# Optimization experiments

Hardware: AMD Instinct MI355X
Metric: run time of the kernel (lower is better)

## Reference

```python
import jax, jax.numpy as jnp
import numpy as np

B, S, D, H = 4, 2048, 1024, 16
DEPTH = D // H
NEG = -1000000000.0


def setup_inputs() -> dict:
    key = jax.random.key(0)
    ks = jax.random.split(key, 11)
    scale = 1.0 / np.sqrt(D)
    return {
        "q": jax.random.normal(ks[0], (B, S, D), jnp.float32),
        "k": jax.random.normal(ks[1], (B, S, D), jnp.float32),
        "v": jax.random.normal(ks[2], (B, S, D), jnp.float32),
        "wq_w": jax.random.normal(ks[3], (D, D), jnp.float32) * scale,
        "wq_b": jax.random.normal(ks[4], (D,), jnp.float32) * 0.01,
        "wk_w": jax.random.normal(ks[5], (D, D), jnp.float32) * scale,
        "wk_b": jax.random.normal(ks[6], (D,), jnp.float32) * 0.01,
        "wv_w": jax.random.normal(ks[7], (D, D), jnp.float32) * scale,
        "wv_b": jax.random.normal(ks[8], (D,), jnp.float32) * 0.01,
        "dense_w": jax.random.normal(ks[9], (D, D), jnp.float32) * scale,
        "dense_b": jax.random.normal(ks[10], (D,), jnp.float32) * 0.01,
    }


def _split_heads(x):
    # (B, S, D) -> (B, H, S, depth)
    b, s, _ = x.shape
    return x.reshape(b, s, H, DEPTH).transpose(0, 2, 1, 3)


def reference(q, k, v, wq_w, wq_b, wk_w, wk_b, wv_w, wv_b, dense_w, dense_b):
    b, s, _ = q.shape
    qh = _split_heads(q @ wq_w.T + wq_b)
    kh = _split_heads(k @ wk_w.T + wk_b)
    vh = _split_heads(v @ wv_w.T + wv_b)
    logits = jnp.einsum('bhqd,bhkd->bhqk', qh, kh) / np.sqrt(DEPTH).astype(np.float32)
    # additive causal mask (strict upper triangle = -1e9)
    mask = jnp.where(jnp.triu(jnp.ones((s, s), jnp.float32), k=1) == 1.0, NEG, 0.0)
    logits = logits + mask
    attn = jax.nn.softmax(logits, axis=-1)
    out = jnp.einsum('bhqk,bhkd->bhqd', attn, vh)
    out = out.transpose(0, 2, 1, 3).reshape(b, s, D)
    return out @ dense_w.T + dense_b
```

## Files before the change

kernel.cpp:

```cpp
#include <hip/hip_runtime.h>
#include <hip/hip_bf16.h>


typedef __attribute__((ext_vector_type(8))) short bf16x8;
typedef __attribute__((ext_vector_type(4))) float f32x4;
typedef __attribute__((ext_vector_type(8))) unsigned short u16x8;

#define MFMA16(a, b, c) __builtin_amdgcn_mfma_f32_16x16x32_bf16(a, b, c, 0, 0, 0)

#define GLOAD_LDS16(gp, lp)                                                    \
  __builtin_amdgcn_global_load_lds(                                            \
      (const __attribute__((address_space(1))) void*)(gp),                     \
      (__attribute__((address_space(3))) void*)(lp), 16, 0, 0)

__device__ __forceinline__ unsigned short f2bf(float f) {
  union { float f; unsigned u; } x; x.f = f;
  unsigned u = x.u;
  return (unsigned short)((u + 0x7fffu + ((u >> 16) & 1u)) >> 16);
}

__device__ __forceinline__ unsigned pk2(float a, float b) {
  union { __hip_bfloat162 h; unsigned u; } cv;
  cv.h = __float22bfloat162_rn(float2{a, b});
  return cv.u;
}

__global__ __launch_bounds__(256) void convert_kernel(
    const float* __restrict__ q, const float* __restrict__ k,
    const float* __restrict__ v, const float* __restrict__ wq,
    const float* __restrict__ wk, const float* __restrict__ wv,
    const float* __restrict__ wd, const float* __restrict__ bq,
    const float* __restrict__ bk, const float* __restrict__ bv,
    unsigned short* __restrict__ dst, float* __restrict__ bias_pack) {
  const size_t tid0 = (size_t)blockIdx.x * blockDim.x + threadIdx.x;
  const size_t nthreads = (size_t)gridDim.x * blockDim.x;
  if (tid0 < 3072) {
    bias_pack[tid0] = tid0 < 1024 ? bq[tid0]
                     : (tid0 < 2048 ? bk[tid0 - 1024] : bv[tid0 - 2048]);
  }
  const size_t NQ = 8192ull * 1024;
  const size_t NW = 1024ull * 1024;
  const size_t total_chunks = (3 * NQ + 4 * NW) / 8;
  for (size_t c = tid0; c < total_chunks; c += nthreads) {
    const size_t e = c * 8;
    const float* src;
    if (e < NQ) src = q + e;
    else if (e < 2 * NQ) src = k + (e - NQ);
    else if (e < 3 * NQ) src = v + (e - 2 * NQ);
    else {
      const size_t we = e - 3 * NQ;
      if (we < NW) src = wq + we;
      else if (we < 2 * NW) src = wk + (we - NW);
      else if (we < 3 * NW) src = wv + (we - 2 * NW);
      else src = wd + (we - 3 * NW);
    }
    f32x4 a = *(const f32x4*)(src);
    f32x4 b = *(const f32x4*)(src + 4);
    u16x8 o;
    o[0] = f2bf(a[0]); o[1] = f2bf(a[1]); o[2] = f2bf(a[2]); o[3] = f2bf(a[3]);
    o[4] = f2bf(b[0]); o[5] = f2bf(b[1]); o[6] = f2bf(b[2]); o[7] = f2bf(b[3]);
    *(u16x8*)(dst + e) = o;
  }
}

template <int MODE>
__global__ __launch_bounds__(512, 2) void gemm8_kernel(
    const unsigned short* __restrict__ Abase,
    const unsigned short* __restrict__ Wbase,
    const float* __restrict__ biasbase, unsigned short* __restrict__ dstb,
    float* __restrict__ dstf) {
  __shared__ __attribute__((aligned(16))) unsigned short Ablk[3][128 * 64];
  __shared__ __attribute__((aligned(16))) unsigned short Bblk[3][256 * 64];
  const size_t NQ = 8192ull * 1024, NW = 1024ull * 1024;
  const int nx = gridDim.x, ny = gridDim.y;
  const int tot = nx * ny * (int)gridDim.z;
  int flat = ((int)blockIdx.z * ny + blockIdx.y) * nx + blockIdx.x;
  flat = (flat & 7) * (tot >> 3) + (flat >> 3);
  const int bx = flat % nx;
  const int tmp = flat / nx;
  const int by = tmp % ny;
  const int z = tmp / ny;

  const unsigned short* A;
  const unsigned short* W;
  if (MODE == 0) { A = Abase + (size_t)z * NQ; W = Wbase + (size_t)z * NW; }
  else if (MODE == 2) { A = Wbase + 2 * NW; W = Abase + 2 * NQ; }
  else { A = Abase; W = Wbase; }
  const int m0 = by * 128, n0 = bx * 256;

  const int tid = threadIdx.x, lane = tid & 63, w = tid >> 6;
  const int wm = w >> 2, wn = w & 3;
  const int llo = lane & 15, lhi = lane >> 4;

  int srcA[2], srcB[4];
#pragma unroll
  for (int j = 0; j < 4; ++j) {
    const int c = tid + j * 512;
    const int off = (c >> 3) * 1024 + ((((c & 7) ^ ((c >> 3) & 7))) << 3);
    if (j < 2) srcA[j] = off;
    srcB[j] = off;
  }
  const unsigned short* Ag = A + (size_t)m0 * 1024;
  const unsigned short* Wg = W + (size_t)n0 * 1024;

#define STA(bi, kt_, j)                                                        \
  GLOAD_LDS16(Ag + srcA[j] + (kt_) * 64,                                       \
              (unsigned short*)Ablk[bi] + (tid + (j) * 512) * 8)
#define STB(bi, kt_, j)                                                        \
  GLOAD_LDS16(Wg + srcB[j] + (kt_) * 64,                                       \
              (unsigned short*)Bblk[bi] + (tid + (j) * 512) * 8)

  f32x4 acc[4][4] = {};
  const int cswz0 = ((lhi ^ (llo & 7)) << 3);
  const int cswz1 = (((4 + lhi) ^ (llo & 7)) << 3);

  STA(0, 0, 0); STA(0, 0, 1);
  STB(0, 0, 0); STB(0, 0, 1); STB(0, 0, 2); STB(0, 0, 3);
  STA(1, 1, 0); STA(1, 1, 1);
  STB(1, 1, 0); STB(1, 1, 1); STB(1, 1, 2); STB(1, 1, 3);

#pragma unroll
  for (int kt = 0; kt < 16; ++kt) {
    const int cb = kt % 3, nb = (kt + 2) % 3;
    __builtin_amdgcn_s_barrier();
    __builtin_amdgcn_sched_barrier(0);
    if (kt + 2 < 16) { STA(nb, kt + 2, 0); STA(nb, kt + 2, 1); STB(nb, kt + 2, 0); }
    if (kt <= 13) asm volatile("s_waitcnt vmcnt(9)" ::: "memory");
    else if (kt == 14) asm volatile("s_waitcnt vmcnt(6)" ::: "memory");
    else asm volatile("s_waitcnt vmcnt(0)" ::: "memory");
    __builtin_amdgcn_s_barrier();
    __builtin_amdgcn_sched_barrier(0);

    bf16x8 af[4][2], bf01[2][2];
#pragma unroll
    for (int mi = 0; mi < 4; ++mi) {
      const int ar = (wm * 64 + mi * 16 + llo) * 64;
      af[mi][0] = *(const bf16x8*)&Ablk[cb][ar + cswz0];
      af[mi][1] = *(const bf16x8*)&Ablk[cb][ar + cswz1];
    }
#pragma unroll
    for (int ni = 0; ni < 2; ++ni) {
      const int br = (wn * 64 + ni * 16 + llo) * 64;
      bf01[ni][0] = *(const bf16x8*)&Bblk[cb][br + cswz0];
      bf01[ni][1] = *(const bf16x8*)&Bblk[cb][br + cswz1];
    }
    __builtin_amdgcn_s_setprio(1);
#pragma unroll
    for (int mi = 0; mi < 4; ++mi)
#pragma unroll
      for (int ni = 0; ni < 2; ++ni) {
        acc[mi][ni] = MFMA16(af[mi][0], bf01[ni][0], acc[mi][ni]);
        acc[mi][ni] = MFMA16(af[mi][1], bf01[ni][1], acc[mi][ni]);
      }
    __builtin_amdgcn_s_setprio(0);
    __builtin_amdgcn_s_barrier();
    __builtin_amdgcn_sched_barrier(0);

    if (kt + 2 < 16) { STB(nb, kt + 2, 1); STB(nb, kt + 2, 2); STB(nb, kt + 2, 3); }
    bf16x8 bf23[2][2];
#pragma unroll
    for (int ni = 0; ni < 2; ++ni) {
      const int br = (wn * 64 + (ni + 2) * 16 + llo) * 64;
      bf23[ni][0] = *(const bf16x8*)&Bblk[cb][br + cswz0];
      bf23[ni][1] = *(const bf16x8*)&Bblk[cb][br + cswz1];
    }
    __builtin_amdgcn_s_setprio(1);
#pragma unroll
    for (int mi = 0; mi < 4; ++mi)
#pragma unroll
      for (int ni = 0; ni < 2; ++ni) {
        acc[mi][ni + 2] = MFMA16(af[mi][0], bf23[ni][0], acc[mi][ni + 2]);
        acc[mi][ni + 2] = MFMA16(af[mi][1], bf23[ni][1], acc[mi][ni + 2]);
      }
    __builtin_amdgcn_s_setprio(0);
  }
#undef STA
#undef STB

  const float osc = (MODE == 0 && z == 0) ? 0.1803368801f : 1.0f;
  const float* bias = (MODE == 0) ? biasbase + (size_t)z * 1024
                     : (MODE == 2) ? biasbase + 2048 : biasbase;
#pragma unroll
  for (int mi = 0; mi < 4; ++mi) {
#pragma unroll
    for (int ni = 0; ni < 4; ++ni) {
      const int n = n0 + wn * 64 + ni * 16 + llo;
      const int mbase = m0 + wm * 64 + mi * 16 + lhi * 4;
#pragma unroll
      for (int r = 0; r < 4; ++r) {
        const int m = mbase + r;
        if (MODE == 1) {
          dstf[(size_t)m * 1024 + n] = acc[mi][ni][r] + bias[n];
        } else if (MODE == 0) {
          const float val = (acc[mi][ni][r] + bias[n]) * osc;
          const int b = m >> 11, s = m & 2047, h = n >> 6, d = n & 63;
          dstb[(size_t)z * NQ + (((size_t)(b * 16 + h) * 2048 + s) * 64 + d)] =
              f2bf(val);
        } else {
          const float val = acc[mi][ni][r] + bias[m];
          const int h = m >> 6, d = m & 63, b = n >> 11, sidx = n & 2047;
          const int t = sidx & 63;
          const int ps = (sidx & ~63) | ((t & 15) << 2) | (t >> 4);
          dstb[2 * NQ + (((size_t)(b * 16 + h) * 64 + d) * 2048 + ps)] =
              f2bf(val);
        }
      }
    }
  }
}

__global__ __launch_bounds__(256, 4) void attn_kernel(
    const unsigned short* __restrict__ Qp, const unsigned short* __restrict__ Kp,
    const unsigned short* __restrict__ Vtp, unsigned short* __restrict__ attn_out) {
  __shared__ __attribute__((aligned(16))) unsigned short Klds[64 * 64];
  __shared__ __attribute__((aligned(16))) unsigned short Vt[80 * 64];
  __shared__ __attribute__((aligned(16))) unsigned short Plds[4 * 32 * 72];
  const int bh = blockIdx.x;
  const int qt = 15 - blockIdx.y;
  const int tid = threadIdx.x, lane = tid & 63, w = tid >> 6;
  const int llo = lane & 15, lhi = lane >> 4;
  const int q0 = qt * 128;
  const int qbase = q0 + w * 32;

  {
    const unsigned v16 = (tid < 16) ? 0x3F80u : 0u;
    const unsigned vv = v16 | (v16 << 16);
    *(uint2*)&Vt[64 * 64 + tid * 4] = make_uint2(vv, vv);
  }

  bf16x8 qf[2][2];
#pragma unroll
  for (int mi = 0; mi < 2; ++mi) {
    const unsigned short* qptr =
        Qp + ((size_t)bh * 2048 + qbase + mi * 16 + llo) * 64 + lhi * 8;
    qf[mi][0] = *(const bf16x8*)qptr;
    qf[mi][1] = *(const bf16x8*)(qptr + 32);
  }

  f32x4 o[2][5] = {};

  const size_t kbase = (size_t)bh * (64 * 2048);
  const int r0 = tid >> 3, r1 = r0 + 32;
  const int scb = (tid & 7) * 16;
  const int kcol0 = (scb ^ ((r0 & 7) << 4)) >> 1;
  const int kcol1 = (scb ^ ((r1 & 7) << 4)) >> 1;
  const int koff0 = r0 * 64 + kcol0, koff1 = r1 * 64 + kcol1;
  const int voff0 = r0 * 2048 + kcol0, voff1 = r1 * 2048 + kcol1;
  unsigned short* pw = &Plds[w * (32 * 72)];

  const int nkt = 2 * (qt + 1);
  for (int kt = 0; kt < nkt; ++kt) {
    const int kv0 = kt * 64;
    if (kt) __syncthreads();
    GLOAD_LDS16(Kp + kbase + (size_t)kv0 * 64 + koff0, &Klds[tid * 8]);
    GLOAD_LDS16(Kp + kbase + (size_t)kv0 * 64 + koff1, &Klds[2048 + tid * 8]);
    GLOAD_LDS16(Vtp + kbase + kv0 + voff0, &Vt[tid * 8]);
    GLOAD_LDS16(Vtp + kbase + kv0 + voff1, &Vt[2048 + tid * 8]);
    __syncthreads();
    if (kv0 > qbase + 31) continue;

    f32x4 s[2][4] = {};
#pragma unroll
    for (int b4 = 0; b4 < 4; ++b4) {
      const int row = b4 * 16 + llo;
      const int sw = (row & 7) << 3;
      const bf16x8 k0 = *(const bf16x8*)&Klds[row * 64 + ((lhi * 8) ^ sw)];
      const bf16x8 k1 = *(const bf16x8*)&Klds[row * 64 + ((32 + lhi * 8) ^ sw)];
      s[0][b4] = MFMA16(qf[0][0], k0, s[0][b4]);
      s[0][b4] = MFMA16(qf[0][1], k1, s[0][b4]);
      s[1][b4] = MFMA16(qf[1][0], k0, s[1][b4]);
      s[1][b4] = MFMA16(qf[1][1], k1, s[1][b4]);
    }

    const bool needm = (kv0 + 63 > qbase);
#pragma unroll
    for (int mi = 0; mi < 2; ++mi) {
#pragma unroll
      for (int r = 0; r < 4; ++r) {
        float sv0 = s[mi][0][r], sv1 = s[mi][1][r];
        float sv2 = s[mi][2][r], sv3 = s[mi][3][r];
        if (needm) {
          const int qrow = qbase + mi * 16 + lhi * 4 + r;
          if (kv0 + llo > qrow) sv0 = -1e9f;
          if (kv0 + 16 + llo > qrow) sv1 = -1e9f;
          if (kv0 + 32 + llo > qrow) sv2 = -1e9f;
          if (kv0 + 48 + llo > qrow) sv3 = -1e9f;
        }
        const float p0 = exp2f(sv0), p1 = exp2f(sv1);
        const float p2 = exp2f(sv2), p3 = exp2f(sv3);
        const int prow = mi * 16 + lhi * 4 + r;
        *(uint2*)&pw[prow * 72 + llo * 4] = make_uint2(pk2(p0, p1), pk2(p2, p3));
      }
    }

    bf16x8 pa[2][2];
#pragma unroll
    for (int mi = 0; mi < 2; ++mi) {
      pa[mi][0] = *(const bf16x8*)&pw[(mi * 16 + llo) * 72 + lhi * 8];
      pa[mi][1] = *(const bf16x8*)&pw[(mi * 16 + llo) * 72 + 32 + lhi * 8];
    }
#pragma unroll
    for (int dblk = 0; dblk < 5; ++dblk) {
      const int row = dblk * 16 + llo;
      const int sw = (row & 7) << 3;
      const bf16x8 v0 = *(const bf16x8*)&Vt[row * 64 + ((lhi * 8) ^ sw)];
      const bf16x8 v1 = *(const bf16x8*)&Vt[row * 64 + ((32 + lhi * 8) ^ sw)];
      o[0][dblk] = MFMA16(pa[0][0], v0, o[0][dblk]);
      o[0][dblk] = MFMA16(pa[0][1], v1, o[0][dblk]);
      o[1][dblk] = MFMA16(pa[1][0], v0, o[1][dblk]);
      o[1][dblk] = MFMA16(pa[1][1], v1, o[1][dblk]);
    }
  }

  const int b = bh >> 4, h = bh & 15;
#pragma unroll
  for (int mi = 0; mi < 2; ++mi) {
#pragma unroll
    for (int r = 0; r < 4; ++r) {
      const float lsum = __shfl(o[mi][4][r], lane & 48);
      const float inv = 1.0f / lsum;
      const int qrow = qbase + mi * 16 + lhi * 4 + r;
      const size_t base = ((size_t)b * 2048 + qrow) * 1024 + h * 64;
#pragma unroll
      for (int dblk = 0; dblk < 4; ++dblk)
        attn_out[base + dblk * 16 + llo] = f2bf(o[mi][dblk][r] * inv);
    }
  }
}

extern "C" void kernel_launch(void* const* d_in, const int* in_sizes, int n_in,
                              void* d_out, int out_size, void* d_ws,
                              size_t ws_size, hipStream_t stream) {
  const float* q = (const float*)d_in[0];
  const float* k = (const float*)d_in[1];
  const float* v = (const float*)d_in[2];
  const float* wq_w = (const float*)d_in[3];
  const float* wq_b = (const float*)d_in[4];
  const float* wk_w = (const float*)d_in[5];
  const float* wk_b = (const float*)d_in[6];
  const float* wv_w = (const float*)d_in[7];
  const float* wv_b = (const float*)d_in[8];
  const float* dense_w = (const float*)d_in[9];
  const float* dense_b = (const float*)d_in[10];
  float* out = (float*)d_out;

  char* ws = (char*)d_ws;
  const size_t MB = 1024ull * 1024;
  unsigned short* qkv_bf = (unsigned short*)(ws);
  unsigned short* w_bf = (unsigned short*)(ws + 48 * MB);
  float* bias_pack = (float*)(ws + 56 * MB);
  unsigned short* qkvp = (unsigned short*)(ws + 57 * MB);
  unsigned short* attn_o = (unsigned short*)(ws + 105 * MB);
  const size_t PEL = 8192ull * 1024;

  convert_kernel<<<dim3(2048), dim3(256), 0, stream>>>(
      q, k, v, wq_w, wk_w, wv_w, dense_w, wq_b, wk_b, wv_b, qkv_bf, bias_pack);

  gemm8_kernel<0><<<dim3(4, 64, 2), dim3(512), 0, stream>>>(
      qkv_bf, w_bf, bias_pack, qkvp, nullptr);

  gemm8_kernel<2><<<dim3(32, 8, 1), dim3(512), 0, stream>>>(
      qkv_bf, w_bf, bias_pack, qkvp, nullptr);

  attn_kernel<<<dim3(64, 16), dim3(256), 0, stream>>>(
      qkvp, qkvp + PEL, qkvp + 2 * PEL, attn_o);

  gemm8_kernel<1><<<dim3(4, 64, 1), dim3(512), 0, stream>>>(
      attn_o, w_bf + 3ull * 1024 * 1024, dense_b, nullptr, out);
}
```

Before: 187.3 us.

## Merge QKV projection launches and overlap K/V tile loads with attention compute

The Q/K and V projection GEMMs are combined into a single 768-block launch that picks the sub-problem from a flat block index, removing one launch and the tail between the two. The attention loop now loads the first K/V tile before the loop. It issues the next K tile's loads after the QK^T/softmax phase and the next V tile's loads after the PV phase, so global-to-LDS copies overlap compute instead of sitting serially at the top of each iteration. This adds a second barrier per iteration and keeps the single-buffer LDS layout, which constrains how much overlap is possible.

Measured after the change: 209.4 us. 11.8% more time.

```diff
diff --git a/kernel.cpp b/kernel.cpp
--- a/kernel.cpp
+++ b/kernel.cpp
@@ -72,21 +72,36 @@
   __shared__ __attribute__((aligned(16))) unsigned short Ablk[3][128 * 64];
   __shared__ __attribute__((aligned(16))) unsigned short Bblk[3][256 * 64];
   const size_t NQ = 8192ull * 1024, NW = 1024ull * 1024;
-  const int nx = gridDim.x, ny = gridDim.y;
-  const int tot = nx * ny * (int)gridDim.z;
-  int flat = ((int)blockIdx.z * ny + blockIdx.y) * nx + blockIdx.x;
+  const int tot = (int)(gridDim.x * gridDim.y);
+  int flat = (int)blockIdx.y * gridDim.x + blockIdx.x;
   flat = (flat & 7) * (tot >> 3) + (flat >> 3);
-  const int bx = flat % nx;
-  const int tmp = flat / nx;
-  const int by = tmp % ny;
-  const int z = tmp / ny;
 
   const unsigned short* A;
   const unsigned short* W;
-  if (MODE == 0) { A = Abase + (size_t)z * NQ; W = Wbase + (size_t)z * NW; }
-  else if (MODE == 2) { A = Wbase + 2 * NW; W = Abase + 2 * NQ; }
-  else { A = Abase; W = Wbase; }
-  const int m0 = by * 128, n0 = bx * 256;
+  int m0, n0, z;
+  if (MODE == 3) {
+    if (flat < 512) {
+      z = flat >> 8;
+      const int rem = flat & 255;
+      m0 = (rem >> 2) * 128;
+      n0 = (rem & 3) * 256;
+      A = Abase + (size_t)z * NQ;
+      W = Wbase + (size_t)z * NW;
+    } else {
+      z = 2;
+      const int i = flat - 512;
+      m0 = (i >> 5) * 128;
+      n0 = (i & 31) * 256;
+      A = Wbase + 2 * NW;
+      W = Abase + 2 * NQ;
+    }
+  } else {
+    z = 0;
+    m0 = (flat >> 2) * 128;
+    n0 = (flat & 3) * 256;
+    A = Abase;
+    W = Wbase;
+  }
 
   const int tid = threadIdx.x, lane = tid & 63, w = tid >> 6;
   const int wm = w >> 2, wn = w & 3;
@@ -177,9 +192,8 @@
 #undef STA
 #undef STB
 
-  const float osc = (MODE == 0 && z == 0) ? 0.1803368801f : 1.0f;
-  const float* bias = (MODE == 0) ? biasbase + (size_t)z * 1024
-                     : (MODE == 2) ? biasbase + 2048 : biasbase;
+  const float osc = (MODE == 3 && z == 0) ? 0.1803368801f : 1.0f;
+  const float* bias = (MODE == 3) ? biasbase + (size_t)z * 1024 : biasbase;
 #pragma unroll
   for (int mi = 0; mi < 4; ++mi) {
 #pragma unroll
@@ -191,7 +205,7 @@
         const int m = mbase + r;
         if (MODE == 1) {
           dstf[(size_t)m * 1024 + n] = acc[mi][ni][r] + bias[n];
-        } else if (MODE == 0) {
+        } else if (z < 2) {
           const float val = (acc[mi][ni][r] + bias[n]) * osc;
           const int b = m >> 11, s = m & 2047, h = n >> 6, d = n & 63;
           dstb[(size_t)z * NQ + (((size_t)(b * 16 + h) * 2048 + s) * 64 + d)] =
@@ -248,69 +262,96 @@
   const int voff0 = r0 * 2048 + kcol0, voff1 = r1 * 2048 + kcol1;
   unsigned short* pw = &Plds[w * (32 * 72)];
 
+#define STAGE_K(kv0_)                                                          \
+  do {                                                                         \
+    GLOAD_LDS16(Kp + kbase + (size_t)(kv0_)*64 + koff0, &Klds[tid * 8]);       \
+    GLOAD_LDS16(Kp + kbase + (size_t)(kv0_)*64 + koff1, &Klds[2048 + tid * 8]);\
+  } while (0)
+#define STAGE_V(kv0_)                                                          \
+  do {                                                                         \
+    GLOAD_LDS16(Vtp + kbase + (kv0_) + voff0, &Vt[tid * 8]);                   \
+    GLOAD_LDS16(Vtp + kbase + (kv0_) + voff1, &Vt[2048 + tid * 8]);            \
+  } while (0)
+
   const int nkt = 2 * (qt + 1);
+  STAGE_K(0);
+  STAGE_V(0);
+  __syncthreads();
+
   for (int kt = 0; kt < nkt; ++kt) {
     const int kv0 = kt * 64;
-    if (kt) __syncthreads();
-    GLOAD_LDS16(Kp + kbase + (size_t)kv0 * 64 + koff0, &Klds[tid * 8]);
-    GLOAD_LDS16(Kp + kbase + (size_t)kv0 * 64 + koff1, &Klds[2048 + tid * 8]);
-    GLOAD_LDS16(Vtp + kbase + kv0 + voff0, &Vt[tid * 8]);
-    GLOAD_LDS16(Vtp + kbase + kv0 + voff1, &Vt[2048 + tid * 8]);
+    const bool act = (kv0 <= qbase + 31);
+
+    f32x4 s[2][4];
+    if (act) {
+#pragma unroll
+      for (int j = 0; j < 2; ++j)
+#pragma unroll
+        for (int b4 = 0; b4 < 4; ++b4) s[j][b4] = f32x4{0.f, 0.f, 0.f, 0.f};
+#pragma unroll
+      for (int b4 = 0; b4 < 4; ++b4) {
+        const int row = b4 * 16 + llo;
+        const int sw = (row & 7) << 3;
+        const bf16x8 k0 = *(const bf16x8*)&Klds[row * 64 + ((lhi * 8) ^ sw)];
+        const bf16x8 k1 = *(const bf16x8*)&Klds[row * 64 + ((32 + lhi * 8) ^ sw)];
+        s[0][b4] = MFMA16(qf[0][0], k0, s[0][b4]);
+        s[0][b4] = MFMA16(qf[0][1], k1, s[0][b4]);
+        s[1][b4] = MFMA16(qf[1][0], k0, s[1][b4]);
+        s[1][b4] = MFMA16(qf[1][1], k1, s[1][b4]);
+      }
+
+      const bool needm = (kv0 + 63 > qbase);
+#pragma unroll
+      for (int mi = 0; mi < 2; ++mi) {
+#pragma unroll
+        for (int r = 0; r < 4; ++r) {
+          float sv0 = s[mi][0][r], sv1 = s[mi][1][r];
+          float sv2 = s[mi][2][r], sv3 = s[mi][3][r];
+          if (needm) {
+            const int qrow = qbase + mi * 16 + lhi * 4 + r;
+            if (kv0 + llo > qrow) sv0 = -1e9f;
+            if (kv0 + 16 + llo > qrow) sv1 = -1e9f;
+            if (kv0 + 32 + llo > qrow) sv2 = -1e9f;
+            if (kv0 + 48 + llo > qrow) sv3 = -1e9f;
+          }
+          const float p0 = exp2f(sv0), p1 = exp2f(sv1);
+          const float p2 = exp2f(sv2), p3 = exp2f(sv3);
+          const int prow = mi * 16 + lhi * 4 + r;
+          *(uint2*)&pw[prow * 72 + llo * 4] =
+              make_uint2(pk2(p0, p1), pk2(p2, p3));
+        }
+      }
+    }
+
     __syncthreads();
-    if (kv0 > qbase + 31) continue;
-
-    f32x4 s[2][4] = {};
-#pragma unroll
-    for (int b4 = 0; b4 < 4; ++b4) {
-      const int row = b4 * 16 + llo;
-      const int sw = (row & 7) << 3;
-      const bf16x8 k0 = *(const bf16x8*)&Klds[row * 64 + ((lhi * 8) ^ sw)];
-      const bf16x8 k1 = *(const bf16x8*)&Klds[row * 64 + ((32 + lhi * 8) ^ sw)];
-      s[0][b4] = MFMA16(qf[0][0], k0, s[0][b4]);
-      s[0][b4] = MFMA16(qf[0][1], k1, s[0][b4]);
-      s[1][b4] = MFMA16(qf[1][0], k0, s[1][b4]);
-      s[1][b4] = MFMA16(qf[1][1], k1, s[1][b4]);
-    }
-
-    const bool needm = (kv0 + 63 > qbase);
-#pragma unroll
-    for (int mi = 0; mi < 2; ++mi) {
-#pragma unroll
-      for (int r = 0; r < 4; ++r) {
-        float sv0 = s[mi][0][r], sv1 = s[mi][1][r];
-        float sv2 = s[mi][2][r], sv3 = s[mi][3][r];
-        if (needm) {
-          const int qrow = qbase + mi * 16 + lhi * 4 + r;
-          if (kv0 + llo > qrow) sv0 = -1e9f;
-          if (kv0 + 16 + llo > qrow) sv1 = -1e9f;
-          if (kv0 + 32 + llo > qrow) sv2 = -1e9f;
-          if (kv0 + 48 + llo > qrow) sv3 = -1e9f;
-        }
-        const float p0 = exp2f(sv0), p1 = exp2f(sv1);
-        const float p2 = exp2f(sv2), p3 = exp2f(sv3);
-        const int prow = mi * 16 + lhi * 4 + r;
-        *(uint2*)&pw[prow * 72 + llo * 4] = make_uint2(pk2(p0, p1), pk2(p2, p3));
-      }
-    }
-
-    bf16x8 pa[2][2];
-#pragma unroll
-    for (int mi = 0; mi < 2; ++mi) {
-      pa[mi][0] = *(const bf16x8*)&pw[(mi * 16 + llo) * 72 + lhi * 8];
-      pa[mi][1] = *(const bf16x8*)&pw[(mi * 16 + llo) * 72 + 32 + lhi * 8];
-    }
-#pragma unroll
-    for (int dblk = 0; dblk < 5; ++dblk) {
-      const int row = dblk * 16 + llo;
-      const int sw = (row & 7) << 3;
-      const bf16x8 v0 = *(const bf16x8*)&Vt[row * 64 + ((lhi * 8) ^ sw)];
-      const bf16x8 v1 = *(const bf16x8*)&Vt[row * 64 + ((32 + lhi * 8) ^ sw)];
-      o[0][dblk] = MFMA16(pa[0][0], v0, o[0][dblk]);
-      o[0][dblk] = MFMA16(pa[0][1], v1, o[0][dblk]);
-      o[1][dblk] = MFMA16(pa[1][0], v0, o[1][dblk]);
-      o[1][dblk] = MFMA16(pa[1][1], v1, o[1][dblk]);
-    }
-  }
+
+    if (kt + 1 < nkt) STAGE_K(kv0 + 64);
+    if (act) {
+      bf16x8 pa[2][2];
+#pragma unroll
+      for (int mi = 0; mi < 2; ++mi) {
+        pa[mi][0] = *(const bf16x8*)&pw[(mi * 16 + llo) * 72 + lhi * 8];
+        pa[mi][1] = *(const bf16x8*)&pw[(mi * 16 + llo) * 72 + 32 + lhi * 8];
+      }
+#pragma unroll
+      for (int dblk = 0; dblk < 5; ++dblk) {
+        const int row = dblk * 16 + llo;
+        const int sw = (row & 7) << 3;
+        const bf16x8 v0 = *(const bf16x8*)&Vt[row * 64 + ((lhi * 8) ^ sw)];
+        const bf16x8 v1 = *(const bf16x8*)&Vt[row * 64 + ((32 + lhi * 8) ^ sw)];
+        o[0][dblk] = MFMA16(pa[0][0], v0, o[0][dblk]);
+        o[0][dblk] = MFMA16(pa[0][1], v1, o[0][dblk]);
+        o[1][dblk] = MFMA16(pa[1][0], v0, o[1][dblk]);
+        o[1][dblk] = MFMA16(pa[1][1], v1, o[1][dblk]);
+      }
+    }
+
+    __syncthreads();
+
+    if (kt + 1 < nkt) STAGE_V(kv0 + 64);
+  }
+#undef STAGE_K
+#undef STAGE_V
 
   const int b = bh >> 4, h = bh & 15;
 #pragma unroll
@@ -356,15 +397,12 @@
   convert_kernel<<<dim3(2048), dim3(256), 0, stream>>>(
       q, k, v, wq_w, wk_w, wv_w, dense_w, wq_b, wk_b, wv_b, qkv_bf, bias_pack);
 
-  gemm8_kernel<0><<<dim3(4, 64, 2), dim3(512), 0, stream>>>(
-      qkv_bf, w_bf, bias_pack, qkvp, nullptr);
-
-  gemm8_kernel<2><<<dim3(32, 8, 1), dim3(512), 0, stream>>>(
+  gemm8_kernel<3><<<dim3(768), dim3(512), 0, stream>>>(
       qkv_bf, w_bf, bias_pack, qkvp, nullptr);
 
   attn_kernel<<<dim3(64, 16), dim3(256), 0, stream>>>(
       qkvp, qkvp + PEL, qkvp + 2 * PEL, attn_o);
 
-  gemm8_kernel<1><<<dim3(4, 64, 1), dim3(512), 0, stream>>>(
+  gemm8_kernel<1><<<dim3(4, 64), dim3(512), 0, stream>>>(
       attn_o, w_bf + 3ull * 1024 * 1024, dense_b, nullptr, out);
 }
```

## Prefetch next K/V tiles into LDS during attention compute phases

Applied to the files above, without the earlier changes.

The attention loop is restructured so the next K tile is issued to LDS right after the QK^T/softmax phase, and the next V tile right after the PV phase. These async global-to-LDS copies now overlap with the other phase's MFMA work instead of stalling at the top of each iteration. The first tile is staged before the loop, and each iteration now has two barriers. This relies on the barrier waiting for the async LDS loads, and it adds synchronisation points that may limit the overlap.

New measurement: 186.8 us. About the same (-0.2%).

```diff
diff --git a/kernel.cpp b/kernel.cpp
--- a/kernel.cpp
+++ b/kernel.cpp
@@ -248,69 +248,96 @@
   const int voff0 = r0 * 2048 + kcol0, voff1 = r1 * 2048 + kcol1;
   unsigned short* pw = &Plds[w * (32 * 72)];
 
+#define STAGE_K(kv0_)                                                          \
+  do {                                                                         \
+    GLOAD_LDS16(Kp + kbase + (size_t)(kv0_)*64 + koff0, &Klds[tid * 8]);       \
+    GLOAD_LDS16(Kp + kbase + (size_t)(kv0_)*64 + koff1, &Klds[2048 + tid * 8]);\
+  } while (0)
+#define STAGE_V(kv0_)                                                          \
+  do {                                                                         \
+    GLOAD_LDS16(Vtp + kbase + (kv0_) + voff0, &Vt[tid * 8]);                   \
+    GLOAD_LDS16(Vtp + kbase + (kv0_) + voff1, &Vt[2048 + tid * 8]);            \
+  } while (0)
+
   const int nkt = 2 * (qt + 1);
+  STAGE_K(0);
+  STAGE_V(0);
+  __syncthreads();
+
   for (int kt = 0; kt < nkt; ++kt) {
     const int kv0 = kt * 64;
-    if (kt) __syncthreads();
-    GLOAD_LDS16(Kp + kbase + (size_t)kv0 * 64 + koff0, &Klds[tid * 8]);
-    GLOAD_LDS16(Kp + kbase + (size_t)kv0 * 64 + koff1, &Klds[2048 + tid * 8]);
-    GLOAD_LDS16(Vtp + kbase + kv0 + voff0, &Vt[tid * 8]);
-    GLOAD_LDS16(Vtp + kbase + kv0 + voff1, &Vt[2048 + tid * 8]);
+    const bool act = (kv0 <= qbase + 31);
+
+    f32x4 s[2][4];
+    if (act) {
+#pragma unroll
+      for (int j = 0; j < 2; ++j)
+#pragma unroll
+        for (int b4 = 0; b4 < 4; ++b4) s[j][b4] = f32x4{0.f, 0.f, 0.f, 0.f};
+#pragma unroll
+      for (int b4 = 0; b4 < 4; ++b4) {
+        const int row = b4 * 16 + llo;
+        const int sw = (row & 7) << 3;
+        const bf16x8 k0 = *(const bf16x8*)&Klds[row * 64 + ((lhi * 8) ^ sw)];
+        const bf16x8 k1 = *(const bf16x8*)&Klds[row * 64 + ((32 + lhi * 8) ^ sw)];
+        s[0][b4] = MFMA16(qf[0][0], k0, s[0][b4]);
+        s[0][b4] = MFMA16(qf[0][1], k1, s[0][b4]);
+        s[1][b4] = MFMA16(qf[1][0], k0, s[1][b4]);
+        s[1][b4] = MFMA16(qf[1][1], k1, s[1][b4]);
+      }
+
+      const bool needm = (kv0 + 63 > qbase);
+#pragma unroll
+      for (int mi = 0; mi < 2; ++mi) {
+#pragma unroll
+        for (int r = 0; r < 4; ++r) {
+          float sv0 = s[mi][0][r], sv1 = s[mi][1][r];
+          float sv2 = s[mi][2][r], sv3 = s[mi][3][r];
+          if (needm) {
+            const int qrow = qbase + mi * 16 + lhi * 4 + r;
+            if (kv0 + llo > qrow) sv0 = -1e9f;
+            if (kv0 + 16 + llo > qrow) sv1 = -1e9f;
+            if (kv0 + 32 + llo > qrow) sv2 = -1e9f;
+            if (kv0 + 48 + llo > qrow) sv3 = -1e9f;
+          }
+          const float p0 = exp2f(sv0), p1 = exp2f(sv1);
+          const float p2 = exp2f(sv2), p3 = exp2f(sv3);
+          const int prow = mi * 16 + lhi * 4 + r;
+          *(uint2*)&pw[prow * 72 + llo * 4] =
+              make_uint2(pk2(p0, p1), pk2(p2, p3));
+        }
+      }
+    }
+
     __syncthreads();
-    if (kv0 > qbase + 31) continue;
-
-    f32x4 s[2][4] = {};
-#pragma unroll
-    for (int b4 = 0; b4 < 4; ++b4) {
-      const int row = b4 * 16 + llo;
-      const int sw = (row & 7) << 3;
-      const bf16x8 k0 = *(const bf16x8*)&Klds[row * 64 + ((lhi * 8) ^ sw)];
-      const bf16x8 k1 = *(const bf16x8*)&Klds[row * 64 + ((32 + lhi * 8) ^ sw)];
-      s[0][b4] = MFMA16(qf[0][0], k0, s[0][b4]);
-      s[0][b4] = MFMA16(qf[0][1], k1, s[0][b4]);
-      s[1][b4] = MFMA16(qf[1][0], k0, s[1][b4]);
-      s[1][b4] = MFMA16(qf[1][1], k1, s[1][b4]);
-    }
-
-    const bool needm = (kv0 + 63 > qbase);
-#pragma unroll
-    for (int mi = 0; mi < 2; ++mi) {
-#pragma unroll
-      for (int r = 0; r < 4; ++r) {
-        float sv0 = s[mi][0][r], sv1 = s[mi][1][r];
-        float sv2 = s[mi][2][r], sv3 = s[mi][3][r];
-        if (needm) {
-          const int qrow = qbase + mi * 16 + lhi * 4 + r;
-          if (kv0 + llo > qrow) sv0 = -1e9f;
-          if (kv0 + 16 + llo > qrow) sv1 = -1e9f;
-          if (kv0 + 32 + llo > qrow) sv2 = -1e9f;
-          if (kv0 + 48 + llo > qrow) sv3 = -1e9f;
-        }
-        const float p0 = exp2f(sv0), p1 = exp2f(sv1);
-        const float p2 = exp2f(sv2), p3 = exp2f(sv3);
-        const int prow = mi * 16 + lhi * 4 + r;
-        *(uint2*)&pw[prow * 72 + llo * 4] = make_uint2(pk2(p0, p1), pk2(p2, p3));
-      }
-    }
-
-    bf16x8 pa[2][2];
-#pragma unroll
-    for (int mi = 0; mi < 2; ++mi) {
-      pa[mi][0] = *(const bf16x8*)&pw[(mi * 16 + llo) * 72 + lhi * 8];
-      pa[mi][1] = *(const bf16x8*)&pw[(mi * 16 + llo) * 72 + 32 + lhi * 8];
-    }
-#pragma unroll
-    for (int dblk = 0; dblk < 5; ++dblk) {
-      const int row = dblk * 16 + llo;
-      const int sw = (row & 7) << 3;
-      const bf16x8 v0 = *(const bf16x8*)&Vt[row * 64 + ((lhi * 8) ^ sw)];
-      const bf16x8 v1 = *(const bf16x8*)&Vt[row * 64 + ((32 + lhi * 8) ^ sw)];
-      o[0][dblk] = MFMA16(pa[0][0], v0, o[0][dblk]);
-      o[0][dblk] = MFMA16(pa[0][1], v1, o[0][dblk]);
-      o[1][dblk] = MFMA16(pa[1][0], v0, o[1][dblk]);
-      o[1][dblk] = MFMA16(pa[1][1], v1, o[1][dblk]);
-    }
-  }
+
+    if (kt + 1 < nkt) STAGE_K(kv0 + 64);
+    if (act) {
+      bf16x8 pa[2][2];
+#pragma unroll
+      for (int mi = 0; mi < 2; ++mi) {
+        pa[mi][0] = *(const bf16x8*)&pw[(mi * 16 + llo) * 72 + lhi * 8];
+        pa[mi][1] = *(const bf16x8*)&pw[(mi * 16 + llo) * 72 + 32 + lhi * 8];
+      }
+#pragma unroll
+      for (int dblk = 0; dblk < 5; ++dblk) {
+        const int row = dblk * 16 + llo;
+        const int sw = (row & 7) << 3;
+        const bf16x8 v0 = *(const bf16x8*)&Vt[row * 64 + ((lhi * 8) ^ sw)];
+        const bf16x8 v1 = *(const bf16x8*)&Vt[row * 64 + ((32 + lhi * 8) ^ sw)];
+        o[0][dblk] = MFMA16(pa[0][0], v0, o[0][dblk]);
+        o[0][dblk] = MFMA16(pa[0][1], v1, o[0][dblk]);
+        o[1][dblk] = MFMA16(pa[1][0], v0, o[1][dblk]);
+        o[1][dblk] = MFMA16(pa[1][1], v1, o[1][dblk]);
+      }
+    }
+
+    __syncthreads();
+
+    if (kt + 1 < nkt) STAGE_V(kv0 + 64);
+  }
+#undef STAGE_K
+#undef STAGE_V
 
   const int b = bh >> 4, h = bh & 15;
 #pragma unroll
@@ -365,6 +392,6 @@
   attn_kernel<<<dim3(64, 16), dim3(256), 0, stream>>>(
       qkvp, qkvp + PEL, qkvp + 2 * PEL, attn_o);
 
-  gemm8_kernel<1><<<dim3(4, 64, 1), dim3(512), 0, stream>>>(
+  gemm8_kernel<1><<<dim3(4, 64), dim3(512), 0, stream>>>(
       attn_o, w_bf + 3ull * 1024 * 1024, dense_b, nullptr, out);
 }
```
